# Optimization experiments

Measured on AMD Instinct MI355X. Metric: run time of the kernel, lower is better.

The kernel has to match this reference:

```python
import jax, jax.numpy as jnp
import numpy as np

N_NODES = 100000
N_EDGES = 2000000


def _mlp3(h, w1, b1, w2, b2, w3, b3):
    h = jax.nn.relu(h @ w1.T + b1)
    h = jax.nn.relu(h @ w2.T + b2)
    return h @ w3.T + b3


def setup_inputs() -> dict:
    key = jax.random.key(0)
    ks = jax.random.split(key, 24)
    inp = {
        "x": jax.random.normal(ks[0], (N_NODES, 3), dtype=jnp.float32),
        "edge_index": jax.random.randint(ks[1], (2, N_EDGES), 0, N_NODES, dtype=jnp.int64),
        "edge_attr": jax.random.normal(ks[2], (N_EDGES, 4), dtype=jnp.float32),
    }
    # MLP params (PyTorch Linear: y = x @ W.T + b)
    shapes = {
        "r1_w1": (40, 10), "r1_b1": (40,), "r1_w2": (40, 40), "r1_b2": (40,), "r1_w3": (4, 40), "r1_b3": (4,),
        "o_w1": (40, 7), "o_b1": (40,), "o_w2": (40, 40), "o_b2": (40,), "o_w3": (3, 40), "o_b3": (3,),
        "r2_w1": (40, 10), "r2_b1": (40,), "r2_w2": (40, 40), "r2_b2": (40,), "r2_w3": (1, 40), "r2_b3": (1,),
    }
    for i, (name, shp) in enumerate(shapes.items()):
        inp[name] = jax.random.normal(ks[3 + i], shp, dtype=jnp.float32) * 0.1
    return inp


def reference(x, edge_index, edge_attr,
              r1_w1, r1_b1, r1_w2, r1_b2, r1_w3, r1_b3,
              o_w1, o_b1, o_w2, o_b2, o_w3, o_b3,
              r2_w1, r2_b1, r2_w2, r2_b2, r2_w3, r2_b3):
    n = x.shape[0]
    src, dst = edge_index[0], edge_index[1]  # x_j <- src, x_i <- dst
    # message: relational MLP R1 over [x_i, x_j, edge_attr]  -> [E,4]
    m1 = jnp.concatenate([x[dst], x[src], edge_attr], axis=1)
    e_msg = _mlp3(m1, r1_w1, r1_b1, r1_w2, r1_b2, r1_w3, r1_b3)
    # aggregate: scatter-add messages to destination nodes -> [N,4]
    aggr = jax.ops.segment_sum(e_msg, dst, num_segments=n)
    # update: object MLP O over [x, aggr] -> [N,3]
    x_tilde = _mlp3(jnp.concatenate([x, aggr], axis=1), o_w1, o_b1, o_w2, o_b2, o_w3, o_b3)
    # edge classifier R2 over [x_tilde_i, x_tilde_j, E] -> sigmoid [E,1]
    m2 = jnp.concatenate([x_tilde[dst], x_tilde[src], e_msg], axis=1)
    return jax.nn.sigmoid(_mlp3(m2, r2_w1, r2_b1, r2_w2, r2_b2, r2_w3, r2_b3))
```

## Files before the change

### kernel.cpp

```cpp
#include <hip/hip_runtime.h>
#include <math.h>


typedef __fp16 hf8 __attribute__((ext_vector_type(8)));
typedef _Float16 f16x2 __attribute__((ext_vector_type(2)));
typedef float f32x16 __attribute__((ext_vector_type(16)));
typedef unsigned u32x4 __attribute__((ext_vector_type(4)));

#define NEPC  64
#define BS    4096
#define NBMAX 32
#define TS    1024

__device__ __forceinline__ f32x16 mfma16(hf8 a, hf8 b, f32x16 c) {
    return __builtin_amdgcn_mfma_f32_32x32x16_f16(a, b, c, 0, 0, 0);
}
__device__ __forceinline__ unsigned pk2(float a, float b) {
    return __builtin_bit_cast(unsigned, __builtin_amdgcn_cvt_pkrtz(a, b));
}
__device__ __forceinline__ unsigned pk2_relu(float a, float b) {
    return __builtin_bit_cast(unsigned,
        __builtin_amdgcn_cvt_pkrtz(fmaxf(a, 0.f), fmaxf(b, 0.f)));
}
__device__ __forceinline__ unsigned pswap(unsigned v) {
    return (unsigned)__shfl_xor((int)v, 32, 64);
}
__device__ __forceinline__ hf8 frag_from(unsigned a, unsigned b, unsigned c, unsigned d) {
    u32x4 v = {a, b, c, d};
    return __builtin_bit_cast(hf8, v);
}

__device__ __forceinline__ void build_frags(const f32x16& t0, const f32x16& t1,
                                            int hi, hf8& F0, hf8& F1, hf8& F2) {
    const unsigned w0 = pk2_relu(t0[0],  t0[1]);
    const unsigned w1 = pk2_relu(t0[2],  t0[3]);
    const unsigned w2 = pk2_relu(t0[4],  t0[5]);
    const unsigned w3 = pk2_relu(t0[6],  t0[7]);
    const unsigned w4 = pk2_relu(t0[8],  t0[9]);
    const unsigned w5 = pk2_relu(t0[10], t0[11]);
    const unsigned w6 = pk2_relu(t0[12], t0[13]);
    const unsigned w7 = pk2_relu(t0[14], t0[15]);
    const unsigned w8 = pk2_relu(t1[0],  t1[1]);
    const unsigned w9 = pk2_relu(t1[2],  t1[3]);
    const unsigned p0 = pswap(w0), p1 = pswap(w1), p2 = pswap(w2), p3 = pswap(w3);
    const unsigned p4 = pswap(w4), p5 = pswap(w5), p6 = pswap(w6), p7 = pswap(w7);
    const unsigned p8 = pswap(w8), p9 = pswap(w9);
    F0 = frag_from(hi ? p2 : w0, hi ? p3 : w1, hi ? w2 : p0, hi ? w3 : p1);
    F1 = frag_from(hi ? p6 : w4, hi ? p7 : w5, hi ? w6 : p4, hi ? w7 : p5);
    F2 = frag_from(hi ? 0x00003c00u : w8, hi ? 0u : w9, hi ? 0u : p8, hi ? 0u : p9);
}

template<int IN, int OUT>
__device__ hf8 load_wfrag(const float* __restrict__ w, const float* __restrict__ b,
                          int mt, int ks, int lane) {
    const int r = mt * 32 + (lane & 31);
    const int kbase = ks * 16 + ((lane >> 5) & 1) * 8;
    hf8 f;
#pragma unroll
    for (int j = 0; j < 8; ++j) {
        const int k = kbase + j;
        float v = 0.f;
        if (r < OUT) {
            if (k < IN) v = w[r * IN + k];
            else if (k == IN) v = b[r];
        }
        f[j] = (__fp16)v;
    }
    return f;
}

template<int OUT>
__device__ hf8 load_wfrag_l1(const float* __restrict__ w, const float* __restrict__ b,
                             int mt, int lane) {
    const int r = mt * 32 + (lane & 31);
    const int kbase = ((lane >> 5) & 1) * 8;
    hf8 f;
#pragma unroll
    for (int j = 0; j < 8; ++j) {
        const int k = kbase + j;
        float v = 0.f;
        if (r < OUT) {
            int src = -1;
            if (k < 3) src = k;
            else if (k >= 4 && k < 7) src = k - 1;
            else if (k >= 8 && k < 12) src = k - 2;
            if (src >= 0) v = w[r * 10 + src];
            else if (k == 12) v = b[r];
        }
        f[j] = (__fp16)v;
    }
    return f;
}

template<bool IS_MSG>
__global__ __launch_bounds__(256, 2) void edge_kernel(
    const uint2* __restrict__ nodef,
    const int*   __restrict__ ei,
    const void*  __restrict__ eattr,
    const float* __restrict__ w1, const float* __restrict__ b1,
    const float* __restrict__ w2, const float* __restrict__ b2,
    const float* __restrict__ w3, const float* __restrict__ b3,
    uint2* __restrict__ emsg_out,
    float* __restrict__ out,
    int n_edges)
{
    const int lane = threadIdx.x & 63;
    const int ecol = lane & 31;
    const int hi = lane >> 5;

    hf8 wa1[2], wa2[2][3], wa3[3];
#pragma unroll
    for (int t = 0; t < 2; ++t) wa1[t] = load_wfrag_l1<40>(w1, b1, t, lane);
#pragma unroll
    for (int t = 0; t < 2; ++t)
#pragma unroll
        for (int s = 0; s < 3; ++s) wa2[t][s] = load_wfrag<40, 40>(w2, b2, t, s, lane);
#pragma unroll
    for (int s = 0; s < 3; ++s)
        wa3[s] = load_wfrag<40, (IS_MSG ? 4 : 1)>(w3, b3, 0, s, lane);

    const int gwave = (int)((blockIdx.x * blockDim.x + threadIdx.x) >> 6);
    const int nwave = (int)((gridDim.x * blockDim.x) >> 6);
    const int nchunk = (n_edges + NEPC - 1) / NEPC;
    const int last = n_edges - 1;

    int c = gwave;
    if (c >= nchunk) return;
    auto eclampX = [&](int cc) { int e = cc * NEPC + ecol;      return e < last ? e : last; };
    auto eclampY = [&](int cc) { int e = cc * NEPC + 32 + ecol; return e < last ? e : last; };

    uint2 fAX, fBX, fAY, fBY;
    int sNX = 0, dNX = 0, sNY = 0, dNY = 0;
    {
        const int eX = eclampX(c), eY = eclampY(c);
        if (hi == 0) {
            const int sX = ei[eX], dX = ei[n_edges + eX];
            const int sY = ei[eY], dY = ei[n_edges + eY];
            fAX = nodef[dX]; fBX = nodef[sX];
            fAY = nodef[dY]; fBY = nodef[sY];
            const int e2X = eclampX(c + nwave), e2Y = eclampY(c + nwave);
            sNX = ei[e2X]; dNX = ei[n_edges + e2X];
            sNY = ei[e2Y]; dNY = ei[n_edges + e2Y];
        } else {
            if (IS_MSG) {
                const float4 evX = ((const float4*)eattr)[eX];
                fAX = make_uint2(pk2(evX.x, evX.y), pk2(evX.z, evX.w));
                const float4 evY = ((const float4*)eattr)[eY];
                fAY = make_uint2(pk2(evY.x, evY.y), pk2(evY.z, evY.w));
            } else {
                fAX = ((const uint2*)eattr)[eX];
                fAY = ((const uint2*)eattr)[eY];
            }
            fBX = make_uint2(0x00003c00u, 0u);
            fBY = fBX;
        }
    }

    for (; c < nchunk; ) {
        const int cn = c + nwave;

        const hf8 bfX = frag_from(fAX.x, fAX.y, fBX.x, fBX.y);
        const hf8 bfY = frag_from(fAY.x, fAY.y, fBY.x, fBY.y);

        uint2 nfAX = fAX, nfBX = fBX, nfAY = fAY, nfBY = fBY;
        int sPX = sNX, dPX = dNX, sPY = sNY, dPY = dNY;
        {
            if (hi == 0) {
                nfAX = nodef[dNX]; nfBX = nodef[sNX];
                nfAY = nodef[dNY]; nfBY = nodef[sNY];
                const int e3X = eclampX(cn + nwave), e3Y = eclampY(cn + nwave);
                sPX = ei[e3X]; dPX = ei[n_edges + e3X];
                sPY = ei[e3Y]; dPY = ei[n_edges + e3Y];
            } else {
                const int e2X = eclampX(cn), e2Y = eclampY(cn);
                if (IS_MSG) {
                    const float4 evX = ((const float4*)eattr)[e2X];
                    nfAX = make_uint2(pk2(evX.x, evX.y), pk2(evX.z, evX.w));
                    const float4 evY = ((const float4*)eattr)[e2Y];
                    nfAY = make_uint2(pk2(evY.x, evY.y), pk2(evY.z, evY.w));
                } else {
                    nfAX = ((const uint2*)eattr)[e2X];
                    nfAY = ((const uint2*)eattr)[e2Y];
                }
            }
        }

        f32x16 a0X = {}, a1X = {}, a0Y = {}, a1Y = {};
        a0X = mfma16(wa1[0], bfX, a0X);
        a0Y = mfma16(wa1[0], bfY, a0Y);
        a1X = mfma16(wa1[1], bfX, a1X);
        a1Y = mfma16(wa1[1], bfY, a1Y);

        hf8 f0X, f1X, f2X, f0Y, f1Y, f2Y;
        build_frags(a0X, a1X, hi, f0X, f1X, f2X);
        build_frags(a0Y, a1Y, hi, f0Y, f1Y, f2Y);

        f32x16 c0X = {}, c1X = {}, c0Y = {}, c1Y = {};
        c0X = mfma16(wa2[0][0], f0X, c0X); c0Y = mfma16(wa2[0][0], f0Y, c0Y);
        c1X = mfma16(wa2[1][0], f0X, c1X); c1Y = mfma16(wa2[1][0], f0Y, c1Y);
        c0X = mfma16(wa2[0][1], f1X, c0X); c0Y = mfma16(wa2[0][1], f1Y, c0Y);
        c1X = mfma16(wa2[1][1], f1X, c1X); c1Y = mfma16(wa2[1][1], f1Y, c1Y);
        c0X = mfma16(wa2[0][2], f2X, c0X); c0Y = mfma16(wa2[0][2], f2Y, c0Y);
        c1X = mfma16(wa2[1][2], f2X, c1X); c1Y = mfma16(wa2[1][2], f2Y, c1Y);

        hf8 g0X, g1X, g2X, g0Y, g1Y, g2Y;
        build_frags(c0X, c1X, hi, g0X, g1X, g2X);
        build_frags(c0Y, c1Y, hi, g0Y, g1Y, g2Y);

        f32x16 z0X = {}, z0Y = {};
        z0X = mfma16(wa3[0], g0X, z0X); z0Y = mfma16(wa3[0], g0Y, z0Y);
        z0X = mfma16(wa3[1], g1X, z0X); z0Y = mfma16(wa3[1], g1Y, z0Y);
        z0X = mfma16(wa3[2], g2X, z0X); z0Y = mfma16(wa3[2], g2Y, z0Y);

        if (hi == 0) {
            const int eX = c * NEPC + ecol;
            const int eY = eX + 32;
            if (eX < n_edges) {
                if (IS_MSG)
                    emsg_out[eX] = make_uint2(pk2(z0X[0], z0X[1]), pk2(z0X[2], z0X[3]));
                else
                    out[eX] = 1.f / (1.f + expf(-z0X[0]));
            }
            if (eY < n_edges) {
                if (IS_MSG)
                    emsg_out[eY] = make_uint2(pk2(z0Y[0], z0Y[1]), pk2(z0Y[2], z0Y[3]));
                else
                    out[eY] = 1.f / (1.f + expf(-z0Y[0]));
            }
        }

        fAX = nfAX; fBX = nfBX; fAY = nfAY; fBY = nfBY;
        sNX = sPX; dNX = dPX; sNY = sPY; dNY = dPY;
        c = cn;
    }
}

__global__ __launch_bounds__(256) void nodef_kernel(
    const float* __restrict__ x, uint2* __restrict__ nodef, int n_nodes)
{
    int n = blockIdx.x * blockDim.x + threadIdx.x;
    if (n >= n_nodes) return;
    nodef[n] = make_uint2(pk2(x[n * 3 + 0], x[n * 3 + 1]), pk2(x[n * 3 + 2], 0.f));
}

__global__ __launch_bounds__(TS) void count_kernel(
    const int* __restrict__ dstp, unsigned* __restrict__ tilecnt, int n_edges)
{
    __shared__ unsigned lc[NBMAX];
    const int tid = threadIdx.x;
    if (tid < NBMAX) lc[tid] = 0u;
    __syncthreads();
    const int e = blockIdx.x * TS + tid;
    if (e < n_edges) atomicAdd(&lc[((unsigned)dstp[e]) >> 12], 1u);
    __syncthreads();
    if (tid < NBMAX) tilecnt[(size_t)blockIdx.x * NBMAX + tid] = lc[tid];
}

__global__ __launch_bounds__(1024) void scan_kernel(
    unsigned* __restrict__ tilecnt, unsigned* __restrict__ totals, int ntiles)
{
    __shared__ unsigned buf[1024];
    const int b = blockIdx.x;
    const int tid = threadIdx.x;
    unsigned carry = 0;
    for (int base = 0; base < ntiles; base += 1024) {
        const int i = base + tid;
        const unsigned v = (i < ntiles) ? tilecnt[(size_t)i * NBMAX + b] : 0u;
        buf[tid] = v;
        __syncthreads();
        for (int off = 1; off < 1024; off <<= 1) {
            const unsigned t = (tid >= off) ? buf[tid - off] : 0u;
            __syncthreads();
            buf[tid] += t;
            __syncthreads();
        }
        if (i < ntiles) tilecnt[(size_t)i * NBMAX + b] = (buf[tid] - v) + carry;
        carry += buf[1023];
        __syncthreads();
    }
    if (tid == 0) totals[b] = carry;
}

__global__ __launch_bounds__(64) void base_kernel(
    const unsigned* __restrict__ totals, unsigned* __restrict__ bases, int nbins)
{
    if (threadIdx.x == 0) {
        unsigned run = 0;
        for (int i = 0; i < nbins; ++i) { bases[i] = run; run += totals[i]; }
    }
}

__global__ __launch_bounds__(TS) void split_kernel(
    const int* __restrict__ dstp,
    const uint2* __restrict__ emsg,
    const unsigned* __restrict__ tilecnt,
    const unsigned* __restrict__ bases,
    unsigned* __restrict__ buckets,
    int n_edges, int nbins)
{
    __shared__ unsigned lcnt[NBMAX], loff[NBMAX], gbase[NBMAX];
    __shared__ unsigned stage[TS * 3];
    const int tid = threadIdx.x;
    const int e = blockIdx.x * TS + tid;
    const bool valid = e < n_edges;

    if (tid < NBMAX) lcnt[tid] = 0u;
    __syncthreads();

    unsigned d = 0, b = 0, slot = 0; uint2 m = make_uint2(0u, 0u);
    if (valid) {
        d = (unsigned)dstp[e];
        m = emsg[e];
        b = d >> 12;
        slot = atomicAdd(&lcnt[b], 1u);
    }
    __syncthreads();

    if (tid < NBMAX && tid < (unsigned)nbins) {
        gbase[tid] = bases[tid] + tilecnt[(size_t)blockIdx.x * NBMAX + tid];
    }
    if (tid == 0) {
        unsigned run = 0;
        for (int i = 0; i < nbins; ++i) { loff[i] = run; run += lcnt[i]; }
    }
    __syncthreads();

    if (valid) {
        const unsigned p = (loff[b] + slot) * 3;
        stage[p] = d; stage[p + 1] = m.x; stage[p + 2] = m.y;
    }
    __syncthreads();

    const int total = min(TS, n_edges - blockIdx.x * TS);
    if (tid < total) {
        const unsigned dd = stage[tid * 3];
        const unsigned bb = dd >> 12;
        const unsigned gpos = gbase[bb] + ((unsigned)tid - loff[bb]);
        unsigned* o = buckets + (size_t)gpos * 3;
        o[0] = dd; o[1] = stage[tid * 3 + 1]; o[2] = stage[tid * 3 + 2];
    }
}

typedef _Float16 hf2 __attribute__((ext_vector_type(2)));
__global__ __launch_bounds__(1024) void accum_kernel(
    const unsigned* __restrict__ buckets,
    const unsigned* __restrict__ totals,
    const unsigned* __restrict__ bases,
    float* __restrict__ scratch,
    int S)
{
    __shared__ float bin[BS * 4];
    const int bid = blockIdx.x / S, s = blockIdx.x % S;
    const int tid = threadIdx.x;

#pragma unroll
    for (int i = 0; i < (BS * 4) / 1024; ++i)
        bin[tid + i * 1024] = 0.f;
    __syncthreads();

    const unsigned start = bases[bid], len = totals[bid];
    const unsigned r0 = start + (unsigned)((unsigned long long)len * s / S);
    const unsigned r1 = start + (unsigned)((unsigned long long)len * (s + 1) / S);
    for (unsigned r = r0 + tid; r < r1; r += 1024) {
        const unsigned* rec = buckets + (size_t)r * 3;
        const unsigned d   = rec[0];
        const unsigned m01 = rec[1];
        const unsigned m23 = rec[2];
        const hf2 lo = __builtin_bit_cast(hf2, m01);
        const hf2 hi = __builtin_bit_cast(hf2, m23);
        float* p = bin + (d & (BS - 1)) * 4;
        atomicAdd(p + 0, (float)lo.x);
        atomicAdd(p + 1, (float)lo.y);
        atomicAdd(p + 2, (float)hi.x);
        atomicAdd(p + 3, (float)hi.y);
    }
    __syncthreads();

    float4* dst = (float4*)(scratch + ((size_t)(bid * S + s)) * BS * 4);
    const float4* srcb = (const float4*)bin;
#pragma unroll
    for (int i = 0; i < (BS * 4) / 4 / 1024; ++i)
        dst[tid + i * 1024] = srcb[tid + i * 1024];
}

__global__ __launch_bounds__(256) void reduce_kernel(
    const float* __restrict__ scratch,
    float* __restrict__ aggr,
    int n_nodes, int nw)
{
    int n = blockIdx.x * blockDim.x + threadIdx.x;
    if (n >= n_nodes) return;
    const int b = n / BS, nl = n % BS;
    float4 acc = make_float4(0.f, 0.f, 0.f, 0.f);
    for (int w = 0; w < nw; ++w) {
        const float4 v = *(const float4*)(scratch + ((size_t)(b * nw + w) * BS + nl) * 4);
        acc.x += v.x; acc.y += v.y; acc.z += v.z; acc.w += v.w;
    }
    *(float4*)(aggr + (size_t)n * 4) = acc;
}

template<int IN, int OUT, bool RELU>
__device__ __forceinline__ void dense(const float* __restrict__ w,
                                      const float* __restrict__ b,
                                      const float* in, float* out) {
#pragma unroll
    for (int j = 0; j < OUT; ++j) {
        float acc = b[j];
#pragma unroll
        for (int k = 0; k < IN; ++k) acc = fmaf(w[j * IN + k], in[k], acc);
        out[j] = RELU ? fmaxf(acc, 0.f) : acc;
    }
}

__global__ __launch_bounds__(256) void node_kernel(
    const float* __restrict__ x,
    const float* __restrict__ aggr,
    const float* __restrict__ w1, const float* __restrict__ b1,
    const float* __restrict__ w2, const float* __restrict__ b2,
    const float* __restrict__ w3, const float* __restrict__ b3,
    uint2* __restrict__ xth,
    int n_nodes)
{
    int n = blockIdx.x * blockDim.x + threadIdx.x;
    if (n >= n_nodes) return;

    float in[7];
    in[0] = x[n * 3 + 0]; in[1] = x[n * 3 + 1]; in[2] = x[n * 3 + 2];
    const float4 ag = *(const float4*)(aggr + (size_t)n * 4);
    in[3] = ag.x; in[4] = ag.y; in[5] = ag.z; in[6] = ag.w;

    float h1[40], h2[40], o[3];
    dense<7, 40, true >(w1, b1, in, h1);
    dense<40, 40, true>(w2, b2, h1, h2);
    dense<40, 3, false>(w3, b3, h2, o);

    xth[n] = make_uint2(pk2(o[0], o[1]), pk2(o[2], 0.f));
}

extern "C" void kernel_launch(void* const* d_in, const int* in_sizes, int n_in,
                              void* d_out, int out_size, void* d_ws, size_t ws_size,
                              hipStream_t stream) {
    const float* x  = (const float*)d_in[0];
    const int*   ei = (const int*)d_in[1];
    const float* ea = (const float*)d_in[2];

    const float* r1_w1 = (const float*)d_in[3];
    const float* r1_b1 = (const float*)d_in[4];
    const float* r1_w2 = (const float*)d_in[5];
    const float* r1_b2 = (const float*)d_in[6];
    const float* r1_w3 = (const float*)d_in[7];
    const float* r1_b3 = (const float*)d_in[8];

    const float* o_w1 = (const float*)d_in[9];
    const float* o_b1 = (const float*)d_in[10];
    const float* o_w2 = (const float*)d_in[11];
    const float* o_b2 = (const float*)d_in[12];
    const float* o_w3 = (const float*)d_in[13];
    const float* o_b3 = (const float*)d_in[14];

    const float* r2_w1 = (const float*)d_in[15];
    const float* r2_b1 = (const float*)d_in[16];
    const float* r2_w2 = (const float*)d_in[17];
    const float* r2_b2 = (const float*)d_in[18];
    const float* r2_w3 = (const float*)d_in[19];
    const float* r2_b3 = (const float*)d_in[20];

    const int n_nodes = in_sizes[0] / 3;
    const int n_edges = in_sizes[2] / 4;
    const int B = (n_nodes + BS - 1) / BS;
    const int ntiles = (n_edges + TS - 1) / TS;

    uint2*    nodef   = (uint2*)d_ws;
    float*    aggr    = (float*)(nodef + n_nodes);
    uint2*    emsg    = (uint2*)(aggr + (size_t)n_nodes * 4);
    unsigned* buckets = (unsigned*)(emsg + n_edges);
    unsigned* totals  = buckets + (size_t)n_edges * 3;
    unsigned* bases   = totals + NBMAX;
    unsigned* tilecnt = bases + NBMAX;
    float*    scratch = (float*)(tilecnt + (size_t)ntiles * NBMAX);

    const size_t fixed_bytes = (char*)scratch - (char*)d_ws;
    int S = 16;
    while (S > 4 && ws_size < fixed_bytes + (size_t)B * S * BS * 4 * sizeof(float))
        S >>= 1;

    const int eb = 512;
    const int nb = (n_nodes + 255) / 256;

    nodef_kernel<<<nb, 256, 0, stream>>>(x, nodef, n_nodes);

    edge_kernel<true><<<eb, 256, 0, stream>>>(nodef, ei, (const void*)ea,
        r1_w1, r1_b1, r1_w2, r1_b2, r1_w3, r1_b3,
        emsg, nullptr, n_edges);

    count_kernel<<<ntiles, TS, 0, stream>>>(ei + n_edges, tilecnt, n_edges);

    scan_kernel<<<B, 1024, 0, stream>>>(tilecnt, totals, ntiles);

    base_kernel<<<1, 64, 0, stream>>>(totals, bases, B);

    split_kernel<<<ntiles, TS, 0, stream>>>(ei + n_edges, emsg, tilecnt, bases,
                                            buckets, n_edges, B);

    accum_kernel<<<B * S, 1024, 0, stream>>>(buckets, totals, bases, scratch, S);

    reduce_kernel<<<nb, 256, 0, stream>>>(scratch, aggr, n_nodes, S);

    node_kernel<<<nb, 256, 0, stream>>>(x, aggr,
        o_w1, o_b1, o_w2, o_b2, o_w3, o_b3, nodef, n_nodes);

    edge_kernel<false><<<eb, 256, 0, stream>>>(nodef, ei, (const void*)emsg,
        r2_w1, r2_b1, r2_w2, r2_b2, r2_w3, r2_b3,
        nullptr, (float*)d_out, n_edges);
}
```

Baseline: 210.1 us.

## Accumulate segment sums in fp16 LDS with packed atomic adds, split bucket layout

Bucket records change from an interleaved 3-word layout to separate dst and packed-message arrays, so loads are coalesced. The per-block LDS bins now hold half-precision sums updated with ds_pk_add_f16: two packed atomics per edge instead of four fp32 atomics. The scratch partials are also written as fp16, which halves scratch traffic, and the reduce kernel converts them back to fp32. The risk is accuracy, since partial sums accumulate in fp16 and can lose precision or overflow.

New measurement: 183.7 us. -12.6%, faster.

```diff
diff --git a/kernel.cpp b/kernel.cpp
--- a/kernel.cpp
+++ b/kernel.cpp
@@ -295,7 +295,8 @@
     const uint2* __restrict__ emsg,
     const unsigned* __restrict__ tilecnt,
     const unsigned* __restrict__ bases,
-    unsigned* __restrict__ buckets,
+    unsigned* __restrict__ bd,
+    uint2* __restrict__ bm,
     int n_edges, int nbins)
 {
     __shared__ unsigned lcnt[NBMAX], loff[NBMAX], gbase[NBMAX];
@@ -336,65 +337,64 @@
         const unsigned dd = stage[tid * 3];
         const unsigned bb = dd >> 12;
         const unsigned gpos = gbase[bb] + ((unsigned)tid - loff[bb]);
-        unsigned* o = buckets + (size_t)gpos * 3;
-        o[0] = dd; o[1] = stage[tid * 3 + 1]; o[2] = stage[tid * 3 + 2];
+        bd[gpos] = dd;
+        bm[gpos] = make_uint2(stage[tid * 3 + 1], stage[tid * 3 + 2]);
     }
 }
 
 typedef _Float16 hf2 __attribute__((ext_vector_type(2)));
 __global__ __launch_bounds__(1024) void accum_kernel(
-    const unsigned* __restrict__ buckets,
+    const unsigned* __restrict__ bd,
+    const uint2* __restrict__ bm,
     const unsigned* __restrict__ totals,
     const unsigned* __restrict__ bases,
-    float* __restrict__ scratch,
+    uint2* __restrict__ scratch,
     int S)
 {
-    __shared__ float bin[BS * 4];
+    __shared__ unsigned bin[BS * 2];
     const int bid = blockIdx.x / S, s = blockIdx.x % S;
     const int tid = threadIdx.x;
 
 #pragma unroll
-    for (int i = 0; i < (BS * 4) / 1024; ++i)
-        bin[tid + i * 1024] = 0.f;
+    for (int i = 0; i < (BS * 2) / 1024; ++i)
+        bin[tid + i * 1024] = 0u;
     __syncthreads();
 
     const unsigned start = bases[bid], len = totals[bid];
     const unsigned r0 = start + (unsigned)((unsigned long long)len * s / S);
     const unsigned r1 = start + (unsigned)((unsigned long long)len * (s + 1) / S);
     for (unsigned r = r0 + tid; r < r1; r += 1024) {
-        const unsigned* rec = buckets + (size_t)r * 3;
-        const unsigned d   = rec[0];
-        const unsigned m01 = rec[1];
-        const unsigned m23 = rec[2];
-        const hf2 lo = __builtin_bit_cast(hf2, m01);
-        const hf2 hi = __builtin_bit_cast(hf2, m23);
-        float* p = bin + (d & (BS - 1)) * 4;
-        atomicAdd(p + 0, (float)lo.x);
-        atomicAdd(p + 1, (float)lo.y);
-        atomicAdd(p + 2, (float)hi.x);
-        atomicAdd(p + 3, (float)hi.y);
-    }
-    __syncthreads();
-
-    float4* dst = (float4*)(scratch + ((size_t)(bid * S + s)) * BS * 4);
-    const float4* srcb = (const float4*)bin;
-#pragma unroll
-    for (int i = 0; i < (BS * 4) / 4 / 1024; ++i)
+        const unsigned d = bd[r];
+        const uint2 m = bm[r];
+        const unsigned laddr =
+            (unsigned)(reinterpret_cast<uintptr_t>(&bin[(d & (BS - 1)) * 2]));
+        asm volatile("ds_pk_add_f16 %0, %1" :: "v"(laddr), "v"(m.x) : "memory");
+        asm volatile("ds_pk_add_f16 %0, %1 offset:4" :: "v"(laddr), "v"(m.y) : "memory");
+    }
+    __syncthreads();
+
+    uint2* dst = scratch + (size_t)(bid * S + s) * BS;
+    const uint2* srcb = (const uint2*)bin;
+#pragma unroll
+    for (int i = 0; i < BS / 1024; ++i)
         dst[tid + i * 1024] = srcb[tid + i * 1024];
 }
 
 __global__ __launch_bounds__(256) void reduce_kernel(
-    const float* __restrict__ scratch,
+    const uint2* __restrict__ scratch,
     float* __restrict__ aggr,
-    int n_nodes, int nw)
+    int n_nodes, int S)
 {
     int n = blockIdx.x * blockDim.x + threadIdx.x;
     if (n >= n_nodes) return;
     const int b = n / BS, nl = n % BS;
     float4 acc = make_float4(0.f, 0.f, 0.f, 0.f);
-    for (int w = 0; w < nw; ++w) {
-        const float4 v = *(const float4*)(scratch + ((size_t)(b * nw + w) * BS + nl) * 4);
-        acc.x += v.x; acc.y += v.y; acc.z += v.z; acc.w += v.w;
+    for (int w = 0; w < S; ++w) {
+        const uint2 v = scratch[(size_t)(b * S + w) * BS + nl];
+        const hf2 lo = __builtin_bit_cast(hf2, v.x);
+        const hf2 hi = __builtin_bit_cast(hf2, v.y);
+        acc.x += (float)lo.x; acc.y += (float)lo.y;
+        acc.z += (float)hi.x; acc.w += (float)hi.y;
     }
     *(float4*)(aggr + (size_t)n * 4) = acc;
 }
@@ -473,15 +473,16 @@
     uint2*    nodef   = (uint2*)d_ws;
     float*    aggr    = (float*)(nodef + n_nodes);
     uint2*    emsg    = (uint2*)(aggr + (size_t)n_nodes * 4);
-    unsigned* buckets = (unsigned*)(emsg + n_edges);
-    unsigned* totals  = buckets + (size_t)n_edges * 3;
+    unsigned* bd      = (unsigned*)(emsg + n_edges);
+    uint2*    bm      = (uint2*)(bd + n_edges);
+    unsigned* totals  = (unsigned*)(bm + n_edges);
     unsigned* bases   = totals + NBMAX;
     unsigned* tilecnt = bases + NBMAX;
-    float*    scratch = (float*)(tilecnt + (size_t)ntiles * NBMAX);
+    uint2*    scratch = (uint2*)(tilecnt + (size_t)ntiles * NBMAX);
 
     const size_t fixed_bytes = (char*)scratch - (char*)d_ws;
     int S = 16;
-    while (S > 4 && ws_size < fixed_bytes + (size_t)B * S * BS * 4 * sizeof(float))
+    while (S > 4 && ws_size < fixed_bytes + (size_t)B * S * BS * sizeof(uint2))
         S >>= 1;
 
     const int eb = 512;
@@ -500,9 +501,9 @@
     base_kernel<<<1, 64, 0, stream>>>(totals, bases, B);
 
     split_kernel<<<ntiles, TS, 0, stream>>>(ei + n_edges, emsg, tilecnt, bases,
-                                            buckets, n_edges, B);
-
-    accum_kernel<<<B * S, 1024, 0, stream>>>(buckets, totals, bases, scratch, S);
+                                            bd, bm, n_edges, B);
+
+    accum_kernel<<<B * S, 1024, 0, stream>>>(bd, bm, totals, bases, scratch, S);
 
     reduce_kernel<<<nb, 256, 0, stream>>>(scratch, aggr, n_nodes, S);
 
```
